# Optimization experiments

Measured on AMD Instinct MI355X. Metric: run time of the kernel, lower is better.

## Reference

```python
import jax, jax.numpy as jnp
import numpy as np
import math

INPUTDIM = 256
OUTDIM = 512
GRIDSIZE = 64

def setup_inputs() -> dict:
    key = jax.random.key(0)
    k1, k2 = jax.random.split(key)
    x = jax.random.normal(k1, (4096, INPUTDIM), dtype=jnp.float32)
    # init: randn / (sqrt(inputdim) * sqrt(gridsize))  (smooth_initialization=False)
    fouriercoeffs = jax.random.normal(k2, (2, OUTDIM, INPUTDIM, GRIDSIZE), dtype=jnp.float32) / (
        math.sqrt(INPUTDIM) * math.sqrt(GRIDSIZE))
    bias = jnp.zeros((1, OUTDIM), dtype=jnp.float32)
    return {"x": x, "fouriercoeffs": fouriercoeffs, "bias": bias}

def reference(x, fouriercoeffs, bias):
    # x: [N, I]; fouriercoeffs: [2, O, I, G]; bias: [1, O]
    k = jnp.arange(1, GRIDSIZE + 1, dtype=x.dtype)          # [G]
    kx = x[:, :, None] * k[None, None, :]                   # [N, I, G]
    c = jnp.cos(kx)
    s = jnp.sin(kx)
    # contraction over (I, G) — GEMM-equivalent of the naive broadcast-sum
    y = jnp.einsum('nig,oig->no', c, fouriercoeffs[0])
    y = y + jnp.einsum('nig,oig->no', s, fouriercoeffs[1])
    y = y + bias
    return y
```

## Files before the change

### kernel.cpp

```cpp
#include <hip/hip_runtime.h>
#include <hip/hip_bf16.h>

#define IDIM 256
#define GDIM 64
#define ODIM 512
#define KD   (IDIM * GDIM)
#define TILE_SHORTS (512 * 64)
#define WS_NEED ((size_t)512 * TILE_SHORTS * 2)

typedef __attribute__((ext_vector_type(8))) short bhalf8;
typedef __attribute__((ext_vector_type(4))) float fvec4;
typedef __attribute__((ext_vector_type(4))) unsigned uvec4;

#define INV2PI 0.15915494309189535f

static __device__ __forceinline__ short bf16b(float v) {
    __hip_bfloat16 hb = __float2bfloat16(v);
    short s; __builtin_memcpy(&s, &hb, 2); return s;
}
static __device__ __forceinline__ unsigned cvtpk(float lo, float hi) {
    unsigned r;
    asm("v_cvt_pk_bf16_f32 %0, %1, %2" : "=v"(r) : "v"(lo), "v"(hi));
    return r;
}

__global__ void prep_b(const float* __restrict__ coeffs, short* __restrict__ ws) {
    const int b = blockIdx.x;
    const int i = b >> 1, h = b & 1;
    const int o = threadIdx.x;
    short* dst = ws + ((size_t)b * 512 + o) * 64;
    const int swz = (o & 7) << 4;
#pragma unroll
    for (int j = 0; j < 8; ++j) {
        const int z = j >> 2, Qq = j & 3;
        const float* src = coeffs + ((size_t)z * ODIM + o) * KD
                         + (size_t)i * GDIM + 16 * Qq + 8 * h;
        fvec4 v0 = ((const fvec4*)src)[0];
        fvec4 v1 = ((const fvec4*)src)[1];
        bhalf8 pk;
#pragma unroll
        for (int u = 0; u < 4; ++u) { pk[u] = bf16b(v0[u]); pk[4 + u] = bf16b(v1[u]); }
        *(bhalf8*)((char*)dst + ((j * 16) ^ swz)) = pk;
    }
}

__global__ void bias_init(const float* __restrict__ bias, float* __restrict__ out) {
    int idx = blockIdx.x * 256 + threadIdx.x;
    fvec4 bv = ((const fvec4*)bias)[idx & 127];
    ((fvec4*)out)[idx] = bv;
}

#define FENCE() do { asm volatile("s_waitcnt vmcnt(0) lgkmcnt(0)" ::: "memory"); \
                     __builtin_amdgcn_sched_barrier(0); \
                     __syncthreads(); } while (0)

template<int USE_WS>
__global__ void __launch_bounds__(256, 4)
fkan_gemm(const float* __restrict__ x, const float* __restrict__ coeffs,
          const short* __restrict__ wsb, float* __restrict__ out) {
    __shared__ __align__(16) short B_lds[2][128 * 64];
    __shared__ float  sl_rev[4][128];
    __shared__ float2 sl_cs[4][128];

    const int bx = blockIdx.x;
    const int xcd = bx & 7, j = bx >> 3;
    const int lg  = xcd * 4 + (j & 3);
    const int mt  = j >> 2;
    const int ot  = lg >> 3, ks = lg & 7;
    const int row0 = mt * 128, col0 = ot * 128;
    const int i0 = ks * 32;

    const int t = threadIdx.x;
    const int lane = t & 63, wid = t >> 6;
    const int wave_m = wid & 1, wave_n = wid >> 1;

    const int rBb = wave_n * 64 + (lane & 15);
    const int kl  = (lane >> 4) * 16;
    const int msk = (lane & 7) << 4;
    const int rA0 = wave_m * 64 + (lane & 15);
    const float m0base = (float)(16 * (lane >> 4) + 1);

    fvec4 acc[4][4];
#pragma unroll
    for (int a = 0; a < 4; ++a)
#pragma unroll
        for (int b = 0; b < 4; ++b) acc[a][b] = (fvec4)0.0f;

    auto fill_sl = [&](int chunk) {
#pragma unroll
        for (int w = 0; w < 2; ++w) {
            int idx = t + w * 256;
            int il2 = idx & 3, r2 = idx >> 2;
            float xv = x[(size_t)(row0 + r2) * IDIM + i0 + chunk * 4 + il2];
            float rev = xv * INV2PI;
            float a = __builtin_amdgcn_fractf(rev);
            float2 cs;
            cs.x = __builtin_amdgcn_cosf(a);
            cs.y = __builtin_amdgcn_sinf(a);
            sl_rev[il2][r2] = rev;
            sl_cs[il2][r2] = cs;
        }
    };

    auto dmaB = [&](int T1) {
        const short* src = wsb + (size_t)(i0 * 2 + T1) * TILE_SHORTS
                         + (size_t)col0 * 64 + (size_t)t * 8;
        const int bsel = T1 & 1;
#pragma unroll
        for (int q = 0; q < 4; ++q)
            __builtin_amdgcn_global_load_lds(
                (const __attribute__((address_space(1))) unsigned*)(src + q * 2048),
                (__attribute__((address_space(3))) unsigned*)
                    &B_lds[bsel][q * 2048 + wid * 512],
                16, 0, 0);
    };

    auto stage_fb = [&](int T1) {
        const int bsel = T1 & 1;
        const int i = i0 + (T1 >> 1), hh = T1 & 1;
        const int o = t >> 1, z = t & 1;
        char* drow = (char*)&B_lds[bsel][o * 64];
        const int swz = (o & 7) << 4;
#pragma unroll
        for (int Qq = 0; Qq < 4; ++Qq) {
            const float* src = coeffs + ((size_t)z * ODIM + col0 + o) * KD
                             + (size_t)i * GDIM + 16 * Qq + 8 * hh;
            fvec4 v0 = ((const fvec4*)src)[0];
            fvec4 v1 = ((const fvec4*)src)[1];
            bhalf8 pk;
#pragma unroll
            for (int u = 0; u < 4; ++u) { pk[u] = bf16b(v0[u]); pk[4 + u] = bf16b(v1[u]); }
            *(bhalf8*)(drow + ((z * 64 + Qq * 16) ^ swz)) = pk;
        }
    };

    fill_sl(0);
    if (USE_WS) dmaB(0);
    FENCE();

#pragma unroll 1
    for (int T = 0; T < 64; ++T) {
        if ((T & 7) == 0 && T > 0) {
            fill_sl(T >> 3);
            FENCE();
        }
        if (USE_WS) {
            if (T < 63) dmaB(T + 1);
            __builtin_amdgcn_sched_barrier(0);
        } else {
            stage_fb(T);
            FENCE();
        }

        const int bsel = T & 1;
        const int il = (T >> 1) & 3;
        const float m0h = m0base + (float)((T & 1) * 8);
        const short* Bb = &B_lds[bsel][0];

        float c_sA[4], c_sB[4], c_C2[4];
        bhalf8 afc[4];
#pragma unroll
        for (int fm = 0; fm < 4; ++fm) {
            const int rr = rA0 + fm * 16;
            float rev = sl_rev[il][rr];
            float2 cs1 = sl_cs[il][rr];
            float C2 = cs1.x + cs1.x;
            float a0 = __builtin_amdgcn_fractf(rev * m0h);
            float c0 = __builtin_amdgcn_cosf(a0);
            float s0 = __builtin_amdgcn_sinf(a0);
            float cA = c0;
            float cB = __builtin_fmaf(c0, cs1.x, -(s0 * cs1.y));
            float sB = __builtin_fmaf(s0, cs1.x,  (c0 * cs1.y));
            c_sA[fm] = s0; c_sB[fm] = sB; c_C2[fm] = C2;
            uvec4 uc;
            uc[0] = cvtpk(cA, cB);
#pragma unroll
            for (int p = 1; p < 4; ++p) {
                float cn = __builtin_fmaf(C2, cB, -cA); cA = cB; cB = cn;
                cn = __builtin_fmaf(C2, cB, -cA); cA = cB; cB = cn;
                uc[p] = cvtpk(cA, cB);
            }
            afc[fm] = __builtin_bit_cast(bhalf8, uc);
        }
        {
            bhalf8 bq[4];
#pragma unroll
            for (int fn = 0; fn < 4; ++fn)
                bq[fn] = *(const bhalf8*)((const char*)Bb +
                    (size_t)(rBb + fn * 16) * 128 + (kl ^ msk));
            __builtin_amdgcn_s_setprio(1);
#pragma unroll
            for (int fm = 0; fm < 4; ++fm)
#pragma unroll
                for (int fn = 0; fn < 4; ++fn)
                    acc[fm][fn] = __builtin_amdgcn_mfma_f32_16x16x32_bf16(
                        afc[fm], bq[fn], acc[fm][fn], 0, 0, 0);
            __builtin_amdgcn_s_setprio(0);
        }

        bhalf8 afs[4];
#pragma unroll
        for (int fm = 0; fm < 4; ++fm) {
            float C2 = c_C2[fm];
            float sA = c_sA[fm], sB = c_sB[fm];
            uvec4 us;
            us[0] = cvtpk(sA, sB);
#pragma unroll
            for (int p = 1; p < 4; ++p) {
                float sn = __builtin_fmaf(C2, sB, -sA); sA = sB; sB = sn;
                sn = __builtin_fmaf(C2, sB, -sA); sA = sB; sB = sn;
                us[p] = cvtpk(sA, sB);
            }
            afs[fm] = __builtin_bit_cast(bhalf8, us);
        }
        {
            bhalf8 bq[4];
#pragma unroll
            for (int fn = 0; fn < 4; ++fn)
                bq[fn] = *(const bhalf8*)((const char*)Bb +
                    (size_t)(rBb + fn * 16) * 128 + ((64 + kl) ^ msk));
            __builtin_amdgcn_s_setprio(1);
#pragma unroll
            for (int fm = 0; fm < 4; ++fm)
#pragma unroll
                for (int fn = 0; fn < 4; ++fn)
                    acc[fm][fn] = __builtin_amdgcn_mfma_f32_16x16x32_bf16(
                        afs[fm], bq[fn], acc[fm][fn], 0, 0, 0);
            __builtin_amdgcn_s_setprio(0);
        }

        FENCE();
    }

#pragma unroll
    for (int fm = 0; fm < 4; ++fm) {
#pragma unroll
        for (int fn = 0; fn < 4; ++fn) {
            int col = col0 + wave_n * 64 + fn * 16 + (lane & 15);
#pragma unroll
            for (int r = 0; r < 4; ++r) {
                int row = row0 + wave_m * 64 + fm * 16 + ((lane >> 4) * 4) + r;
                atomicAdd(&out[(size_t)row * ODIM + col], acc[fm][fn][r]);
            }
        }
    }
}

extern "C" void kernel_launch(void* const* d_in, const int* in_sizes, int n_in,
                              void* d_out, int out_size, void* d_ws, size_t ws_size,
                              hipStream_t stream) {
    (void)in_sizes; (void)n_in; (void)out_size;
    const float* x      = (const float*)d_in[0];
    const float* coeffs = (const float*)d_in[1];
    const float* bias   = (const float*)d_in[2];
    float* out = (float*)d_out;

    const bool use_ws = (ws_size >= WS_NEED) && (((uintptr_t)d_ws & 15) == 0);

    bias_init<<<dim3(2048), dim3(256), 0, stream>>>(bias, out);
    if (use_ws) {
        prep_b<<<dim3(512), dim3(512), 0, stream>>>(coeffs, (short*)d_ws);
        fkan_gemm<1><<<dim3(1024), dim3(256), 0, stream>>>(x, coeffs, (const short*)d_ws, out);
    } else {
        fkan_gemm<0><<<dim3(1024), dim3(256), 0, stream>>>(x, coeffs, nullptr, out);
    }
}
```

Measured before the change: 196.3 us.

## Split waves along M only and carry Chebyshev recurrence across T steps

Changes the wave layout from a 2x2 split of the 128x128 tile to a 4x1 split. Each wave now owns 32 rows and all 128 columns, so it generates only 2 A fragments instead of 4 and each wave's sin/cos generation work is halved. On odd T steps the recurrence state from the even step is reused instead of calling cos/sin again, cutting transcendental work further. The cost is twice as many B fragment LDS reads per wave and a longer serial recurrence chain, which may let bf16 error build up over 16 steps.

```diff
diff --git a/kernel.cpp b/kernel.cpp
--- a/kernel.cpp
+++ b/kernel.cpp
@@ -54,6 +54,12 @@
                      __builtin_amdgcn_sched_barrier(0); \
                      __syncthreads(); } while (0)
 
+#define ADV2(cA,cB,sA,sB,C2) do { \
+    float _cn = __builtin_fmaf((C2),(cB),-(cA)); (cA)=(cB); (cB)=_cn; \
+    float _sn = __builtin_fmaf((C2),(sB),-(sA)); (sA)=(sB); (sB)=_sn; \
+    _cn = __builtin_fmaf((C2),(cB),-(cA)); (cA)=(cB); (cB)=_cn; \
+    _sn = __builtin_fmaf((C2),(sB),-(sA)); (sA)=(sB); (sB)=_sn; } while (0)
+
 template<int USE_WS>
 __global__ void __launch_bounds__(256, 4)
 fkan_gemm(const float* __restrict__ x, const float* __restrict__ coeffs,
@@ -72,19 +78,16 @@
 
     const int t = threadIdx.x;
     const int lane = t & 63, wid = t >> 6;
-    const int wave_m = wid & 1, wave_n = wid >> 1;
-
-    const int rBb = wave_n * 64 + (lane & 15);
     const int kl  = (lane >> 4) * 16;
     const int msk = (lane & 7) << 4;
-    const int rA0 = wave_m * 64 + (lane & 15);
-    const float m0base = (float)(16 * (lane >> 4) + 1);
-
-    fvec4 acc[4][4];
-#pragma unroll
-    for (int a = 0; a < 4; ++a)
-#pragma unroll
-        for (int b = 0; b < 4; ++b) acc[a][b] = (fvec4)0.0f;
+    const int rA0 = wid * 32 + (lane & 15);
+    const float m0f = (float)(16 * (lane >> 4) + 1);
+
+    fvec4 acc[2][8];
+#pragma unroll
+    for (int a = 0; a < 2; ++a)
+#pragma unroll
+        for (int b = 0; b < 8; ++b) acc[a][b] = (fvec4)0.0f;
 
     auto fill_sl = [&](int chunk) {
 #pragma unroll
@@ -138,6 +141,9 @@
     if (USE_WS) dmaB(0);
     FENCE();
 
+    float ccA0, ccB0, csA0, csB0, cC20;
+    float ccA1, ccB1, csA1, csB1, cC21;
+
 #pragma unroll 1
     for (int T = 0; T < 64; ++T) {
         if ((T & 7) == 0 && T > 0) {
@@ -154,78 +160,76 @@
 
         const int bsel = T & 1;
         const int il = (T >> 1) & 3;
-        const float m0h = m0base + (float)((T & 1) * 8);
         const short* Bb = &B_lds[bsel][0];
 
-        float c_sA[4], c_sB[4], c_C2[4];
-        bhalf8 afc[4];
-#pragma unroll
-        for (int fm = 0; fm < 4; ++fm) {
-            const int rr = rA0 + fm * 16;
-            float rev = sl_rev[il][rr];
-            float2 cs1 = sl_cs[il][rr];
-            float C2 = cs1.x + cs1.x;
-            float a0 = __builtin_amdgcn_fractf(rev * m0h);
-            float c0 = __builtin_amdgcn_cosf(a0);
-            float s0 = __builtin_amdgcn_sinf(a0);
-            float cA = c0;
-            float cB = __builtin_fmaf(c0, cs1.x, -(s0 * cs1.y));
-            float sB = __builtin_fmaf(s0, cs1.x,  (c0 * cs1.y));
-            c_sA[fm] = s0; c_sB[fm] = sB; c_C2[fm] = C2;
-            uvec4 uc;
-            uc[0] = cvtpk(cA, cB);
-#pragma unroll
-            for (int p = 1; p < 4; ++p) {
-                float cn = __builtin_fmaf(C2, cB, -cA); cA = cB; cB = cn;
-                cn = __builtin_fmaf(C2, cB, -cA); cA = cB; cB = cn;
-                uc[p] = cvtpk(cA, cB);
+        bhalf8 afc[2], afs[2];
+        if ((T & 1) == 0) {
+#pragma unroll
+            for (int fm = 0; fm < 2; ++fm) {
+                const int rr = rA0 + fm * 16;
+                float rev = sl_rev[il][rr];
+                float2 cs1 = sl_cs[il][rr];
+                float C2 = cs1.x + cs1.x;
+                float a0 = __builtin_amdgcn_fractf(rev * m0f);
+                float cA = __builtin_amdgcn_cosf(a0);
+                float sA = __builtin_amdgcn_sinf(a0);
+                float cB = __builtin_fmaf(cA, cs1.x, -(sA * cs1.y));
+                float sB = __builtin_fmaf(sA, cs1.x,  (cA * cs1.y));
+                uvec4 uc, us;
+                uc[0] = cvtpk(cA, cB); us[0] = cvtpk(sA, sB);
+#pragma unroll
+                for (int p = 1; p < 4; ++p) {
+                    ADV2(cA, cB, sA, sB, C2);
+                    uc[p] = cvtpk(cA, cB); us[p] = cvtpk(sA, sB);
+                }
+                if (fm == 0) { ccA0 = cA; ccB0 = cB; csA0 = sA; csB0 = sB; cC20 = C2; }
+                else         { ccA1 = cA; ccB1 = cB; csA1 = sA; csB1 = sB; cC21 = C2; }
+                afc[fm] = __builtin_bit_cast(bhalf8, uc);
+                afs[fm] = __builtin_bit_cast(bhalf8, us);
             }
-            afc[fm] = __builtin_bit_cast(bhalf8, uc);
-        }
-        {
+        } else {
+#pragma unroll
+            for (int fm = 0; fm < 2; ++fm) {
+                float cA = fm ? ccA1 : ccA0, cB = fm ? ccB1 : ccB0;
+                float sA = fm ? csA1 : csA0, sB = fm ? csB1 : csB0;
+                float C2 = fm ? cC21 : cC20;
+                uvec4 uc, us;
+#pragma unroll
+                for (int p = 0; p < 4; ++p) {
+                    ADV2(cA, cB, sA, sB, C2);
+                    uc[p] = cvtpk(cA, cB); us[p] = cvtpk(sA, sB);
+                }
+                afc[fm] = __builtin_bit_cast(bhalf8, uc);
+                afs[fm] = __builtin_bit_cast(bhalf8, us);
+            }
+        }
+
+#pragma unroll
+        for (int half = 0; half < 2; ++half) {
             bhalf8 bq[4];
 #pragma unroll
-            for (int fn = 0; fn < 4; ++fn)
-                bq[fn] = *(const bhalf8*)((const char*)Bb +
-                    (size_t)(rBb + fn * 16) * 128 + (kl ^ msk));
+            for (int f4 = 0; f4 < 4; ++f4)
+                bq[f4] = *(const bhalf8*)((const char*)Bb +
+                    (size_t)(half * 64 + f4 * 16 + (lane & 15)) * 128 + (kl ^ msk));
             __builtin_amdgcn_s_setprio(1);
 #pragma unroll
-            for (int fm = 0; fm < 4; ++fm)
-#pragma unroll
-                for (int fn = 0; fn < 4; ++fn)
-                    acc[fm][fn] = __builtin_amdgcn_mfma_f32_16x16x32_bf16(
-                        afc[fm], bq[fn], acc[fm][fn], 0, 0, 0);
+            for (int fm = 0; fm < 2; ++fm)
+#pragma unroll
+                for (int f4 = 0; f4 < 4; ++f4)
+                    acc[fm][half * 4 + f4] = __builtin_amdgcn_mfma_f32_16x16x32_bf16(
+                        afc[fm], bq[f4], acc[fm][half * 4 + f4], 0, 0, 0);
             __builtin_amdgcn_s_setprio(0);
-        }
-
-        bhalf8 afs[4];
-#pragma unroll
-        for (int fm = 0; fm < 4; ++fm) {
-            float C2 = c_C2[fm];
-            float sA = c_sA[fm], sB = c_sB[fm];
-            uvec4 us;
-            us[0] = cvtpk(sA, sB);
-#pragma unroll
-            for (int p = 1; p < 4; ++p) {
-                float sn = __builtin_fmaf(C2, sB, -sA); sA = sB; sB = sn;
-                sn = __builtin_fmaf(C2, sB, -sA); sA = sB; sB = sn;
-                us[p] = cvtpk(sA, sB);
-            }
-            afs[fm] = __builtin_bit_cast(bhalf8, us);
-        }
-        {
-            bhalf8 bq[4];
-#pragma unroll
-            for (int fn = 0; fn < 4; ++fn)
-                bq[fn] = *(const bhalf8*)((const char*)Bb +
-                    (size_t)(rBb + fn * 16) * 128 + ((64 + kl) ^ msk));
+#pragma unroll
+            for (int f4 = 0; f4 < 4; ++f4)
+                bq[f4] = *(const bhalf8*)((const char*)Bb +
+                    (size_t)(half * 64 + f4 * 16 + (lane & 15)) * 128 + ((64 + kl) ^ msk));
             __builtin_amdgcn_s_setprio(1);
 #pragma unroll
-            for (int fm = 0; fm < 4; ++fm)
-#pragma unroll
-                for (int fn = 0; fn < 4; ++fn)
-                    acc[fm][fn] = __builtin_amdgcn_mfma_f32_16x16x32_bf16(
-                        afs[fm], bq[fn], acc[fm][fn], 0, 0, 0);
+            for (int fm = 0; fm < 2; ++fm)
+#pragma unroll
+                for (int f4 = 0; f4 < 4; ++f4)
+                    acc[fm][half * 4 + f4] = __builtin_amdgcn_mfma_f32_16x16x32_bf16(
+                        afs[fm], bq[f4], acc[fm][half * 4 + f4], 0, 0, 0);
             __builtin_amdgcn_s_setprio(0);
         }
 
@@ -233,14 +237,14 @@
     }
 
 #pragma unroll
-    for (int fm = 0; fm < 4; ++fm) {
-#pragma unroll
-        for (int fn = 0; fn < 4; ++fn) {
-            int col = col0 + wave_n * 64 + fn * 16 + (lane & 15);
+    for (int fm = 0; fm < 2; ++fm) {
+#pragma unroll
+        for (int f = 0; f < 8; ++f) {
+            int col = col0 + f * 16 + (lane & 15);
 #pragma unroll
             for (int r = 0; r < 4; ++r) {
-                int row = row0 + wave_m * 64 + fm * 16 + ((lane >> 4) * 4) + r;
-                atomicAdd(&out[(size_t)row * ODIM + col], acc[fm][fn][r]);
+                int row = row0 + wid * 32 + fm * 16 + ((lane >> 4) * 4) + r;
+                atomicAdd(&out[(size_t)row * ODIM + col], acc[fm][f][r]);
             }
         }
     }
```

Result: faster. 176.7 us (-10.0%).

## Drop LDS staging, load B fragments directly to registers, double split-K

Applied to the files above, without the earlier changes.

Removes shared memory entirely. B fragments are now read straight from the pre-swizzled workspace into registers with a two-deep register double buffer, and x values are loaded per lane with sin/cos computed inline instead of through an LDS table. That eliminates all barriers and waitcnt fences in the main loop. Split-K is doubled to 16 chunks of 16 input dims, with 2048 blocks and launch bounds lowered to 3. The cost is higher register pressure, redundant global loads of B across waves (no LDS sharing between wave_m pairs), and twice as many atomic adds into the output.

```diff
diff --git a/kernel.cpp b/kernel.cpp
--- a/kernel.cpp
+++ b/kernel.cpp
@@ -6,6 +6,7 @@
 #define ODIM 512
 #define KD   (IDIM * GDIM)
 #define TILE_SHORTS (512 * 64)
+#define TILE_BYTES  (TILE_SHORTS * 2)
 #define WS_NEED ((size_t)512 * TILE_SHORTS * 2)
 
 typedef __attribute__((ext_vector_type(8))) short bhalf8;
@@ -23,6 +24,9 @@
     asm("v_cvt_pk_bf16_f32 %0, %1, %2" : "=v"(r) : "v"(lo), "v"(hi));
     return r;
 }
+
+#define ADVP(A,B,C2) do { float _t = __builtin_fmaf((C2),(B),-(A)); (A)=(B); (B)=_t; \
+                          _t = __builtin_fmaf((C2),(B),-(A)); (A)=(B); (B)=_t; } while (0)
 
 __global__ void prep_b(const float* __restrict__ coeffs, short* __restrict__ ws) {
     const int b = blockIdx.x;
@@ -50,35 +54,26 @@
     ((fvec4*)out)[idx] = bv;
 }
 
-#define FENCE() do { asm volatile("s_waitcnt vmcnt(0) lgkmcnt(0)" ::: "memory"); \
-                     __builtin_amdgcn_sched_barrier(0); \
-                     __syncthreads(); } while (0)
-
 template<int USE_WS>
-__global__ void __launch_bounds__(256, 4)
+__global__ void __launch_bounds__(256, 3)
 fkan_gemm(const float* __restrict__ x, const float* __restrict__ coeffs,
           const short* __restrict__ wsb, float* __restrict__ out) {
-    __shared__ __align__(16) short B_lds[2][128 * 64];
-    __shared__ float  sl_rev[4][128];
-    __shared__ float2 sl_cs[4][128];
-
     const int bx = blockIdx.x;
     const int xcd = bx & 7, j = bx >> 3;
-    const int lg  = xcd * 4 + (j & 3);
-    const int mt  = j >> 2;
-    const int ot  = lg >> 3, ks = lg & 7;
+    const int lg  = xcd * 8 + (j & 7);
+    const int mt  = j >> 3;
+    const int ot  = lg >> 4, ks = lg & 15;
     const int row0 = mt * 128, col0 = ot * 128;
-    const int i0 = ks * 32;
+    const int i0 = ks * 16;
 
     const int t = threadIdx.x;
     const int lane = t & 63, wid = t >> 6;
     const int wave_m = wid & 1, wave_n = wid >> 1;
-
-    const int rBb = wave_n * 64 + (lane & 15);
     const int kl  = (lane >> 4) * 16;
     const int msk = (lane & 7) << 4;
     const int rA0 = wave_m * 64 + (lane & 15);
-    const float m0base = (float)(16 * (lane >> 4) + 1);
+    const int cB0 = wave_n * 64 + (lane & 15);
+    const float m0f = (float)(16 * (lane >> 4) + 1);
 
     fvec4 acc[4][4];
 #pragma unroll
@@ -86,150 +81,133 @@
 #pragma unroll
         for (int b = 0; b < 4; ++b) acc[a][b] = (fvec4)0.0f;
 
-    auto fill_sl = [&](int chunk) {
-#pragma unroll
-        for (int w = 0; w < 2; ++w) {
-            int idx = t + w * 256;
-            int il2 = idx & 3, r2 = idx >> 2;
-            float xv = x[(size_t)(row0 + r2) * IDIM + i0 + chunk * 4 + il2];
-            float rev = xv * INV2PI;
-            float a = __builtin_amdgcn_fractf(rev);
-            float2 cs;
-            cs.x = __builtin_amdgcn_cosf(a);
-            cs.y = __builtin_amdgcn_sinf(a);
-            sl_rev[il2][r2] = rev;
-            sl_cs[il2][r2] = cs;
+    int boff[2][4];
+#pragma unroll
+    for (int z = 0; z < 2; ++z)
+#pragma unroll
+        for (int fn = 0; fn < 4; ++fn)
+            boff[z][fn] = (cB0 + fn * 16) * 128 + ((z * 64 + kl) ^ msk);
+
+    const char* wsb0 = (const char*)wsb + (size_t)(i0 * 2) * TILE_BYTES
+                     + (size_t)col0 * 128;
+    const float* xb = x + (size_t)(row0 + rA0) * IDIM + i0;
+
+    bhalf8 bq0[8], bq1[8];
+
+    auto loadB = [&](bhalf8* bq, int T) {
+        if (USE_WS) {
+            const char* tb = wsb0 + (size_t)T * TILE_BYTES;
+#pragma unroll
+            for (int z = 0; z < 2; ++z)
+#pragma unroll
+                for (int fn = 0; fn < 4; ++fn)
+                    bq[z * 4 + fn] = *(const bhalf8*)(tb + boff[z][fn]);
+        } else {
+            const int i = i0 + (T >> 1), h = T & 1, Q = lane >> 4;
+#pragma unroll
+            for (int z = 0; z < 2; ++z)
+#pragma unroll
+                for (int fn = 0; fn < 4; ++fn) {
+                    const float* f = coeffs
+                        + ((size_t)z * ODIM + col0 + cB0 + fn * 16) * KD
+                        + (size_t)i * GDIM + 16 * Q + 8 * h;
+                    fvec4 v0 = ((const fvec4*)f)[0];
+                    fvec4 v1 = ((const fvec4*)f)[1];
+                    uvec4 u;
+                    u[0] = cvtpk(v0[0], v0[1]); u[1] = cvtpk(v0[2], v0[3]);
+                    u[2] = cvtpk(v1[0], v1[1]); u[3] = cvtpk(v1[2], v1[3]);
+                    bq[z * 4 + fn] = __builtin_bit_cast(bhalf8, u);
+                }
         }
     };
 
-    auto dmaB = [&](int T1) {
-        const short* src = wsb + (size_t)(i0 * 2 + T1) * TILE_SHORTS
-                         + (size_t)col0 * 64 + (size_t)t * 8;
-        const int bsel = T1 & 1;
-#pragma unroll
-        for (int q = 0; q < 4; ++q)
-            __builtin_amdgcn_global_load_lds(
-                (const __attribute__((address_space(1))) unsigned*)(src + q * 2048),
-                (__attribute__((address_space(3))) unsigned*)
-                    &B_lds[bsel][q * 2048 + wid * 512],
-                16, 0, 0);
-    };
-
-    auto stage_fb = [&](int T1) {
-        const int bsel = T1 & 1;
-        const int i = i0 + (T1 >> 1), hh = T1 & 1;
-        const int o = t >> 1, z = t & 1;
-        char* drow = (char*)&B_lds[bsel][o * 64];
-        const int swz = (o & 7) << 4;
-#pragma unroll
-        for (int Qq = 0; Qq < 4; ++Qq) {
-            const float* src = coeffs + ((size_t)z * ODIM + col0 + o) * KD
-                             + (size_t)i * GDIM + 16 * Qq + 8 * hh;
-            fvec4 v0 = ((const fvec4*)src)[0];
-            fvec4 v1 = ((const fvec4*)src)[1];
-            bhalf8 pk;
-#pragma unroll
-            for (int u = 0; u < 4; ++u) { pk[u] = bf16b(v0[u]); pk[4 + u] = bf16b(v1[u]); }
-            *(bhalf8*)(drow + ((z * 64 + Qq * 16) ^ swz)) = pk;
-        }
-    };
-
-    fill_sl(0);
-    if (USE_WS) dmaB(0);
-    FENCE();
+    float kcA[4], kcB[4], ksA[4], ksB[4], kC2[4];
+    float xv[4];
+
+    loadB(bq0, 0);
+#pragma unroll
+    for (int fm = 0; fm < 4; ++fm) xv[fm] = xb[fm * 16 * IDIM];
 
 #pragma unroll 1
-    for (int T = 0; T < 64; ++T) {
-        if ((T & 7) == 0 && T > 0) {
-            fill_sl(T >> 3);
-            FENCE();
-        }
-        if (USE_WS) {
-            if (T < 63) dmaB(T + 1);
-            __builtin_amdgcn_sched_barrier(0);
-        } else {
-            stage_fb(T);
-            FENCE();
-        }
-
-        const int bsel = T & 1;
-        const int il = (T >> 1) & 3;
-        const float m0h = m0base + (float)((T & 1) * 8);
-        const short* Bb = &B_lds[bsel][0];
-
-        float c_sA[4], c_sB[4], c_C2[4];
-        bhalf8 afc[4];
+    for (int ii = 0; ii < 16; ++ii) {
+        loadB(bq1, 2 * ii + 1);
 #pragma unroll
         for (int fm = 0; fm < 4; ++fm) {
-            const int rr = rA0 + fm * 16;
-            float rev = sl_rev[il][rr];
-            float2 cs1 = sl_cs[il][rr];
-            float C2 = cs1.x + cs1.x;
-            float a0 = __builtin_amdgcn_fractf(rev * m0h);
+            float rev = xv[fm] * INV2PI;
+            float a1 = __builtin_amdgcn_fractf(rev);
+            float c1 = __builtin_amdgcn_cosf(a1);
+            float s1 = __builtin_amdgcn_sinf(a1);
+            float C2x = c1 + c1;
+            float a0 = __builtin_amdgcn_fractf(rev * m0f);
             float c0 = __builtin_amdgcn_cosf(a0);
             float s0 = __builtin_amdgcn_sinf(a0);
-            float cA = c0;
-            float cB = __builtin_fmaf(c0, cs1.x, -(s0 * cs1.y));
-            float sB = __builtin_fmaf(s0, cs1.x,  (c0 * cs1.y));
-            c_sA[fm] = s0; c_sB[fm] = sB; c_C2[fm] = C2;
-            uvec4 uc;
-            uc[0] = cvtpk(cA, cB);
-#pragma unroll
-            for (int p = 1; p < 4; ++p) {
-                float cn = __builtin_fmaf(C2, cB, -cA); cA = cB; cB = cn;
-                cn = __builtin_fmaf(C2, cB, -cA); cA = cB; cB = cn;
-                uc[p] = cvtpk(cA, cB);
-            }
-            afc[fm] = __builtin_bit_cast(bhalf8, uc);
-        }
-        {
-            bhalf8 bq[4];
-#pragma unroll
-            for (int fn = 0; fn < 4; ++fn)
-                bq[fn] = *(const bhalf8*)((const char*)Bb +
-                    (size_t)(rBb + fn * 16) * 128 + (kl ^ msk));
-            __builtin_amdgcn_s_setprio(1);
-#pragma unroll
-            for (int fm = 0; fm < 4; ++fm)
-#pragma unroll
-                for (int fn = 0; fn < 4; ++fn)
-                    acc[fm][fn] = __builtin_amdgcn_mfma_f32_16x16x32_bf16(
-                        afc[fm], bq[fn], acc[fm][fn], 0, 0, 0);
-            __builtin_amdgcn_s_setprio(0);
-        }
-
-        bhalf8 afs[4];
+            float cBv = __builtin_fmaf(c0, c1, -(s0 * s1));
+            float sBv = __builtin_fmaf(s0, c1, c0 * s1);
+            uvec4 uc, us;
+            uc[0] = cvtpk(c0, cBv);
+            us[0] = cvtpk(s0, sBv);
+            {
+                float A = c0, B = cBv;
+                ADVP(A, B, C2x); uc[1] = cvtpk(A, B);
+                ADVP(A, B, C2x); uc[2] = cvtpk(A, B);
+                ADVP(A, B, C2x); uc[3] = cvtpk(A, B);
+                kcA[fm] = A; kcB[fm] = B;
+            }
+            {
+                float A = s0, B = sBv;
+                ADVP(A, B, C2x); us[1] = cvtpk(A, B);
+                ADVP(A, B, C2x); us[2] = cvtpk(A, B);
+                ADVP(A, B, C2x); us[3] = cvtpk(A, B);
+                ksA[fm] = A; ksB[fm] = B;
+            }
+            kC2[fm] = C2x;
+            bhalf8 afc = __builtin_bit_cast(bhalf8, uc);
+            bhalf8 afs = __builtin_bit_cast(bhalf8, us);
+#pragma unroll
+            for (int fn = 0; fn < 4; ++fn)
+                acc[fm][fn] = __builtin_amdgcn_mfma_f32_16x16x32_bf16(
+                    afc, bq0[fn], acc[fm][fn], 0, 0, 0);
+#pragma unroll
+            for (int fn = 0; fn < 4; ++fn)
+                acc[fm][fn] = __builtin_amdgcn_mfma_f32_16x16x32_bf16(
+                    afs, bq0[4 + fn], acc[fm][fn], 0, 0, 0);
+        }
+
+        const bool more = (ii < 15);
+        if (more) {
+            loadB(bq0, 2 * ii + 2);
+#pragma unroll
+            for (int fm = 0; fm < 4; ++fm) xv[fm] = xb[fm * 16 * IDIM + ii + 1];
+        }
 #pragma unroll
         for (int fm = 0; fm < 4; ++fm) {
-            float C2 = c_C2[fm];
-            float sA = c_sA[fm], sB = c_sB[fm];
-            uvec4 us;
-            us[0] = cvtpk(sA, sB);
-#pragma unroll
-            for (int p = 1; p < 4; ++p) {
-                float sn = __builtin_fmaf(C2, sB, -sA); sA = sB; sB = sn;
-                sn = __builtin_fmaf(C2, sB, -sA); sA = sB; sB = sn;
-                us[p] = cvtpk(sA, sB);
-            }
-            afs[fm] = __builtin_bit_cast(bhalf8, us);
-        }
-        {
-            bhalf8 bq[4];
-#pragma unroll
-            for (int fn = 0; fn < 4; ++fn)
-                bq[fn] = *(const bhalf8*)((const char*)Bb +
-                    (size_t)(rBb + fn * 16) * 128 + ((64 + kl) ^ msk));
-            __builtin_amdgcn_s_setprio(1);
-#pragma unroll
-            for (int fm = 0; fm < 4; ++fm)
-#pragma unroll
-                for (int fn = 0; fn < 4; ++fn)
-                    acc[fm][fn] = __builtin_amdgcn_mfma_f32_16x16x32_bf16(
-                        afs[fm], bq[fn], acc[fm][fn], 0, 0, 0);
-            __builtin_amdgcn_s_setprio(0);
-        }
-
-        FENCE();
+            float C2x = kC2[fm];
+            uvec4 uc, us;
+            {
+                float A = kcA[fm], B = kcB[fm];
+                ADVP(A, B, C2x); uc[0] = cvtpk(A, B);
+                ADVP(A, B, C2x); uc[1] = cvtpk(A, B);
+                ADVP(A, B, C2x); uc[2] = cvtpk(A, B);
+                ADVP(A, B, C2x); uc[3] = cvtpk(A, B);
+            }
+            {
+                float A = ksA[fm], B = ksB[fm];
+                ADVP(A, B, C2x); us[0] = cvtpk(A, B);
+                ADVP(A, B, C2x); us[1] = cvtpk(A, B);
+                ADVP(A, B, C2x); us[2] = cvtpk(A, B);
+                ADVP(A, B, C2x); us[3] = cvtpk(A, B);
+            }
+            bhalf8 afc = __builtin_bit_cast(bhalf8, uc);
+            bhalf8 afs = __builtin_bit_cast(bhalf8, us);
+#pragma unroll
+            for (int fn = 0; fn < 4; ++fn)
+                acc[fm][fn] = __builtin_amdgcn_mfma_f32_16x16x32_bf16(
+                    afc, bq1[fn], acc[fm][fn], 0, 0, 0);
+#pragma unroll
+            for (int fn = 0; fn < 4; ++fn)
+                acc[fm][fn] = __builtin_amdgcn_mfma_f32_16x16x32_bf16(
+                    afs, bq1[4 + fn], acc[fm][fn], 0, 0, 0);
+        }
     }
 
 #pragma unroll
@@ -260,8 +238,8 @@
     bias_init<<<dim3(2048), dim3(256), 0, stream>>>(bias, out);
     if (use_ws) {
         prep_b<<<dim3(512), dim3(512), 0, stream>>>(coeffs, (short*)d_ws);
-        fkan_gemm<1><<<dim3(1024), dim3(256), 0, stream>>>(x, coeffs, (const short*)d_ws, out);
+        fkan_gemm<1><<<dim3(2048), dim3(256), 0, stream>>>(x, coeffs, (const short*)d_ws, out);
     } else {
-        fkan_gemm<0><<<dim3(1024), dim3(256), 0, stream>>>(x, coeffs, nullptr, out);
-    }
-}
+        fkan_gemm<0><<<dim3(2048), dim3(256), 0, stream>>>(x, coeffs, nullptr, out);
+    }
+}
```

Result: slower. 299.5 us (+52.6%).
